# Kernel optimization log

Measured on AMD Instinct MI355X. Metric: run time of the kernel, lower is better.

## Reference

```python
import jax, jax.numpy as jnp
import numpy as np

N_NODES = 50000
EMB = 256
HEADS = 2
N_BASE_EDGES = 100000


def setup_inputs() -> dict:
    key = jax.random.key(0)
    ks = jax.random.split(key, 12)
    x = jax.random.normal(ks[0], (N_NODES, EMB), dtype=jnp.float32)
    # bipartite edges: sources in left half, targets in right half -> no self-loops
    src = jax.random.randint(ks[1], (N_BASE_EDGES,), 0, N_NODES // 2)
    dst = jax.random.randint(ks[2], (N_BASE_EDGES,), N_NODES // 2, N_NODES)
    edge_index = jnp.stack([src, dst]).astype(jnp.int64)
    hd = EMB // HEADS
    s = 0.02
    params = {
        "Wkqv": jax.random.normal(ks[3], (EMB, 3 * EMB), dtype=jnp.float32) * s,
        "bkqv": jnp.zeros((3 * EMB,), dtype=jnp.float32),
        "W1": jax.random.normal(ks[4], (2 * hd, hd), dtype=jnp.float32) * s,
        "b1": jnp.zeros((hd,), dtype=jnp.float32),
        "W2": jax.random.normal(ks[5], (hd, 1), dtype=jnp.float32) * s,
        "b2": jnp.zeros((1,), dtype=jnp.float32),
        "Wout": jax.random.normal(ks[6], (EMB, EMB), dtype=jnp.float32) * s,
        "bout": jnp.zeros((EMB,), dtype=jnp.float32),
    }
    return {"x": x, "edge_index": edge_index, **params}


def reference(x, edge_index, Wkqv, bkqv, W1, b1, W2, b2, Wout, bout):
    N, emb = x.shape
    H = HEADS
    hd = emb // H
    # MetaGNNNoEdgeAttr.forward preprocessing: make undirected + self loops.
    # Input is bipartite (no self-loops), so remove_self_loops is a no-op.
    ei = jnp.concatenate([edge_index, edge_index[::-1]], axis=1)
    loops = jnp.arange(N, dtype=edge_index.dtype)
    src = jnp.concatenate([ei[0], loops])  # j (message source)
    dst = jnp.concatenate([ei[1], loops])  # i (message target / softmax index)

    # single GNN layer (n_layers=1)
    kqv = x @ Wkqv + bkqv  # [N, 3*emb]
    q = kqv[dst, :emb].reshape(-1, H, hd)                                  # [E,H,hd]
    k = kqv[src, emb:2 * emb].reshape(-1, H, hd) / jnp.sqrt(jnp.float32(hd))
    v = kqv[src, 2 * emb:].reshape(-1, H, hd)

    h = jax.nn.relu(jnp.concatenate([k, q], axis=-1) @ W1 + b1)  # [E,H,hd]
    a = (h @ W2 + b2).squeeze(-1)                                # [E,H]

    # segment softmax over destination nodes (every node has a self-loop)
    m = jax.ops.segment_max(a, dst, num_segments=N)              # [N,H]
    ex = jnp.exp(a - m[dst])
    s = jax.ops.segment_sum(ex, dst, num_segments=N)             # [N,H]
    alpha = ex / (s[dst] + 1e-16)                                # [E,H]

    msg = (alpha[..., None] * v).reshape(-1, emb) @ Wout + bout  # [E,emb]
    out = jax.ops.segment_sum(msg, dst, num_segments=N)          # [N,emb]
    return jax.nn.relu(out) + x
```

## Files before the change

### kernel.cpp

```cpp
#include <hip/hip_runtime.h>
#include <hip/hip_bf16.h>

#define EMB 256

typedef __bf16 bf16_t;
typedef __attribute__((ext_vector_type(8))) __bf16 bf16x8;
typedef __attribute__((ext_vector_type(4))) __bf16 bf16x4;
typedef __attribute__((ext_vector_type(4))) float floatx4;

__device__ __forceinline__ int eidx(const int* __restrict__ p, int is64, long long k){
  return is64 ? p[2*k] : p[(int)k];
}
__device__ __forceinline__ void async_load16(const void* g, void* l){
  __builtin_amdgcn_global_load_lds(
      (const __attribute__((address_space(1))) unsigned int*)g,
      (__attribute__((address_space(3))) unsigned int*)l,
      16, 0, 0);
}
__device__ __forceinline__ float4 cvt4(bf16x4 v){
  return make_float4((float)v.x, (float)v.y, (float)v.z, (float)v.w);
}

__global__ void detect_kernel(const int* __restrict__ ei, int* __restrict__ flag){
  int z = (ei[1]==0) + (ei[3]==0) + (ei[5]==0) + (ei[7]==0);
  *flag = (z == 4) ? 1 : 0;
}

__global__ void cvt_x_kernel(const float* __restrict__ x, bf16_t* __restrict__ xb, int n4){
  int t = blockIdx.x*blockDim.x + threadIdx.x;
  if (t >= n4) return;
  const float4 v = *(const float4*)(x + (size_t)t*4);
  bf16x4 o = { (bf16_t)v.x, (bf16_t)v.y, (bf16_t)v.z, (bf16_t)v.w };
  *(bf16x4*)(xb + (size_t)t*4) = o;
}

__global__ void prep_weights(const float* __restrict__ Wkqv, const float* __restrict__ bkqv,
                             const float* __restrict__ W1,
                             bf16_t* __restrict__ WcombT, float* __restrict__ bcomb){
  int n = blockIdx.x * blockDim.x + threadIdx.x;
  int c = blockIdx.y;
  if (n >= 768) return;
  const float rs = rsqrtf(128.0f);
  bool isBias = (c == 256);
  const float* arow = isBias ? bkqv : (Wkqv + (size_t)c*768);
  float val;
  if (n < 256){
    int h = n >> 7, d = n & 127;
    float s = 0.f;
    for (int t = 0; t < 128; ++t)
      s = fmaf(arow[h*128 + t], W1[(size_t)(128 + t)*128 + d], s);
    val = s;
  } else {
    int r = n - 256;
    int h = r >> 8, t8 = r & 255;
    int g = t8 >> 3, half = (t8 >> 2) & 1, dd = t8 & 3;
    int d = g*4 + dd;
    if (half == 0){
      float s = 0.f;
      for (int t = 0; t < 128; ++t)
        s = fmaf(arow[256 + h*128 + t], W1[(size_t)t*128 + d], s);
      val = s * rs;
    } else {
      val = arow[512 + h*128 + d];
    }
  }
  if (isBias) bcomb[n] = val;
  else        WcombT[(size_t)n*256 + c] = (bf16_t)val;
}

__global__ void prep_wout(const float* __restrict__ W, bf16_t* __restrict__ Wt){
  int t = blockIdx.x*blockDim.x + threadIdx.x;
  int n = t & 255, c = t >> 8;
  Wt[(size_t)n*256 + c] = (bf16_t)W[(size_t)c*256 + n];
}

__global__ void deg_kernel(const int* __restrict__ ei, const int* __restrict__ flag,
                           int* __restrict__ deg, int E0, int Nn){
  int t = blockIdx.x*blockDim.x + threadIdx.x;
  if (t >= 2*E0) return;
  int is64 = *flag;
  int i = (t < E0) ? eidx(ei,is64,(long long)E0+t) : eidx(ei,is64,t-E0);
  i = min(max(i,0), Nn-1);
  atomicAdd(deg + i, 1);
}

__global__ __launch_bounds__(1024) void scan1_kernel(const int* __restrict__ deg,
                                                     int* __restrict__ off,
                                                     int* __restrict__ bsum, int N){
  __shared__ int wsum[16];
  int tid = threadIdx.x, lane = tid & 63, w = tid >> 6;
  int i = blockIdx.x*1024 + tid;
  int v = (i < N) ? (deg[i] + 1) : 0;
  int incl = v;
  #pragma unroll
  for (int o = 1; o < 64; o <<= 1){
    int t = __shfl_up(incl, o, 64);
    if (lane >= o) incl += t;
  }
  if (lane == 63) wsum[w] = incl;
  __syncthreads();
  if (w == 0 && lane < 16){
    int sv = wsum[lane];
    #pragma unroll
    for (int o = 1; o < 16; o <<= 1){
      int t = __shfl_up(sv, o, 64);
      if (lane >= o) sv += t;
    }
    wsum[lane] = sv;
  }
  __syncthreads();
  int wpref = (w == 0) ? 0 : wsum[w-1];
  if (i < N) off[i] = wpref + incl - v;
  if (tid == 1023) bsum[blockIdx.x] = wpref + incl;
}

__global__ __launch_bounds__(1024) void scan2_kernel(int* __restrict__ bsum,
                                                     int* __restrict__ off, int nb, int N){
  __shared__ int wsum[16];
  int tid = threadIdx.x, lane = tid & 63, w = tid >> 6;
  int v = (tid < nb) ? bsum[tid] : 0;
  int incl = v;
  #pragma unroll
  for (int o = 1; o < 64; o <<= 1){
    int t = __shfl_up(incl, o, 64);
    if (lane >= o) incl += t;
  }
  if (lane == 63) wsum[w] = incl;
  __syncthreads();
  if (w == 0 && lane < 16){
    int sv = wsum[lane];
    #pragma unroll
    for (int o = 1; o < 16; o <<= 1){
      int t = __shfl_up(sv, o, 64);
      if (lane >= o) sv += t;
    }
    wsum[lane] = sv;
  }
  __syncthreads();
  int wpref = (w == 0) ? 0 : wsum[w-1];
  if (tid < nb) bsum[tid] = wpref + incl - v;
  if (tid == 1023) off[N] = wpref + incl;
}

__global__ void scan3_kernel(int* __restrict__ off, const int* __restrict__ bsum, int N){
  int i = blockIdx.x*256 + threadIdx.x;
  if (i < N) off[i] += bsum[i >> 10];
}

__global__ void scatter_kernel(const int* __restrict__ ei, const int* __restrict__ flag,
                               const int* __restrict__ off, int* __restrict__ cursor,
                               int* __restrict__ bj, int E0, int Nn){
  int e = blockIdx.x*blockDim.x + threadIdx.x;
  int E = 2*E0 + Nn;
  if (e >= E) return;
  int is64 = *flag;
  int j, i;
  if (e < E0){ j = eidx(ei,is64,e); i = eidx(ei,is64,(long long)E0+e); }
  else if (e < 2*E0){ int t = e - E0; i = eidx(ei,is64,t); j = eidx(ei,is64,(long long)E0+t); }
  else { i = j = e - 2*E0; }
  i = min(max(i,0), Nn-1); j = min(max(j,0), Nn-1);
  int pos = atomicAdd(cursor + i, 1);
  bj[off[i] + pos] = j;
}

template<int MODE, typename OutT>
__global__ __launch_bounds__(256) void mfma_gemm(
    const bf16_t* __restrict__ A, const bf16_t* __restrict__ Bt,
    const float* __restrict__ bias, OutT* __restrict__ C,
    int M, int N,
    const int* __restrict__ deg, const float* __restrict__ xres)
{
  __shared__ bf16_t As[2][128*32];
  __shared__ bf16_t Bs[2][128*32];
  const int tid = threadIdx.x;
  const int wave = tid >> 6, lane = tid & 63;
  const int row16 = lane & 15, quad = lane >> 4;

  const int nn = N >> 7;
  const int bid = blockIdx.x;
  const int strip = bid / (8*nn);
  const int inner = bid % (8*nn);
  const int m0 = (strip*8 + (inner & 7)) * 128;
  const int n0 = (inner >> 3) * 128;
  const int wm = (wave >> 1) * 64, wn = (wave & 1) * 64;

  const int f0 = wave*2, f1 = wave*2 + 1;
  const int gm0 = min(m0 + f0*16 + row16, M-1);
  const int gm1 = min(m0 + f1*16 + row16, M-1);
  const int gn0 = n0 + f0*16 + row16;
  const int gn1 = n0 + f1*16 + row16;

  async_load16(A  + (size_t)gm0*256 + quad*8, (char*)As[0] + f0*1024);
  async_load16(A  + (size_t)gm1*256 + quad*8, (char*)As[0] + f1*1024);
  async_load16(Bt + (size_t)gn0*256 + quad*8, (char*)Bs[0] + f0*1024);
  async_load16(Bt + (size_t)gn1*256 + quad*8, (char*)Bs[0] + f1*1024);

  floatx4 acc[4][4];
  #pragma unroll
  for (int a=0;a<4;++a)
    #pragma unroll
    for (int b=0;b<4;++b) acc[a][b] = (floatx4){0.f,0.f,0.f,0.f};

  #pragma unroll
  for (int kt = 0; kt < 8; ++kt){
    const int cur = kt & 1, nxt = cur ^ 1;
    const int k1 = (kt+1)*32;

    __syncthreads();

    if (kt < 7){
      async_load16(A  + (size_t)gm0*256 + k1 + quad*8, (char*)As[nxt] + f0*1024);
      async_load16(A  + (size_t)gm1*256 + k1 + quad*8, (char*)As[nxt] + f1*1024);
      async_load16(Bt + (size_t)gn0*256 + k1 + quad*8, (char*)Bs[nxt] + f0*1024);
      async_load16(Bt + (size_t)gn1*256 + k1 + quad*8, (char*)Bs[nxt] + f1*1024);
    }

    bf16x8 af[4], bfr[4];
    #pragma unroll
    for (int t = 0; t < 4; ++t){
      af[t]  = *(const bf16x8*)((const char*)As[cur] + ((wm>>4)+t)*1024 + lane*16);
      bfr[t] = *(const bf16x8*)((const char*)Bs[cur] + ((wn>>4)+t)*1024 + lane*16);
    }
    #pragma unroll
    for (int mt=0;mt<4;++mt)
      #pragma unroll
      for (int nt=0;nt<4;++nt)
        acc[mt][nt] = __builtin_amdgcn_mfma_f32_16x16x32_bf16(bfr[nt], af[mt], acc[mt][nt], 0,0,0);
  }

  float4 b4[4];
  #pragma unroll
  for (int nt=0;nt<4;++nt)
    b4[nt] = *(const float4*)(bias + n0 + wn + nt*16 + quad*4);

  #pragma unroll
  for (int mt=0;mt<4;++mt){
    const int m = m0 + wm + mt*16 + row16;
    if (m >= M) continue;
    const float dg = (MODE==1) ? (float)(deg[m]+1) : 0.f;
    #pragma unroll
    for (int nt=0;nt<4;++nt){
      const int nb = n0 + wn + nt*16 + quad*4;
      if (MODE == 0){
        bf16x4 o = { (bf16_t)(acc[mt][nt][0] + b4[nt].x),
                     (bf16_t)(acc[mt][nt][1] + b4[nt].y),
                     (bf16_t)(acc[mt][nt][2] + b4[nt].z),
                     (bf16_t)(acc[mt][nt][3] + b4[nt].w) };
        *(bf16x4*)((bf16_t*)C + (size_t)m*N + nb) = o;
      } else {
        const float4 xr = *(const float4*)(xres + (size_t)m*N + nb);
        float4 o;
        o.x = fmaxf(acc[mt][nt][0] + dg*b4[nt].x, 0.f) + xr.x;
        o.y = fmaxf(acc[mt][nt][1] + dg*b4[nt].y, 0.f) + xr.y;
        o.z = fmaxf(acc[mt][nt][2] + dg*b4[nt].z, 0.f) + xr.z;
        o.w = fmaxf(acc[mt][nt][3] + dg*b4[nt].w, 0.f) + xr.w;
        *(float4*)((float*)C + (size_t)m*N + nb) = o;
      }
    }
  }
}

__device__ __forceinline__ float score4(bf16x8 kvv, float4 qv, float4 b1v, float4 w2v){
  return fmaxf(qv.x+(float)kvv[0]+b1v.x, 0.f)*w2v.x
       + fmaxf(qv.y+(float)kvv[1]+b1v.y, 0.f)*w2v.y
       + fmaxf(qv.z+(float)kvv[2]+b1v.z, 0.f)*w2v.z
       + fmaxf(qv.w+(float)kvv[3]+b1v.w, 0.f)*w2v.w;
}
__device__ __forceinline__ float hredux(float p){
  #pragma unroll
  for (int o = 16; o >= 1; o >>= 1)
    p += __shfl_xor(p, o, 64);
  return p;
}
__global__ __launch_bounds__(256) void fused_attn_kernel(
    const bf16_t* __restrict__ P, const int* __restrict__ bj, const int* __restrict__ off,
    const float* __restrict__ b1, const float* __restrict__ W2, const float* __restrict__ b2,
    bf16_t* __restrict__ aggb, int Nn)
{
  int i = blockIdx.x * (blockDim.x >> 6) + (threadIdx.x >> 6);
  if (i >= Nn) return;
  int lane = threadIdx.x & 63;
  int h = lane >> 5, g = lane & 31, d = g * 4;

  const float4 qv  = cvt4(*(const bf16x4*)(P + (size_t)i*768 + h*128 + d));
  const float4 b1v = *(const float4*)(b1 + d);
  const float4 w2v = *(const float4*)(W2 + d);
  const float b2v  = b2[0];
  const bf16_t* __restrict__ Pkv = P + 256 + h*256 + g*8;

  float m = -3.0e38f, s = 0.f;
  float4 acc = make_float4(0.f,0.f,0.f,0.f);
  const int s0 = off[i], s1 = off[i+1], s1m1 = s1 - 1;

  for (int t = s0; t < s1; t += 4){
    const int cnt = s1 - t;
    const int jA = bj[t];
    const int jB = bj[min(t+1, s1m1)];
    const int jC = bj[min(t+2, s1m1)];
    const int jD = bj[min(t+3, s1m1)];
    const bf16x8 kA = *(const bf16x8*)(Pkv + (size_t)jA*768);
    const bf16x8 kB = *(const bf16x8*)(Pkv + (size_t)jB*768);
    const bf16x8 kC = *(const bf16x8*)(Pkv + (size_t)jC*768);
    const bf16x8 kD = *(const bf16x8*)(Pkv + (size_t)jD*768);
    float pA = hredux(score4(kA, qv, b1v, w2v));
    float pB = hredux(score4(kB, qv, b1v, w2v));
    float pC = hredux(score4(kC, qv, b1v, w2v));
    float pD = hredux(score4(kD, qv, b1v, w2v));
    const float aA = pA + b2v;
    const float aB = (cnt > 1) ? pB + b2v : -3.0e38f;
    const float aC = (cnt > 2) ? pC + b2v : -3.0e38f;
    const float aD = (cnt > 3) ? pD + b2v : -3.0e38f;
    const float amax = fmaxf(fmaxf(aA, aB), fmaxf(aC, aD));
    const float mn = fmaxf(m, amax);
    const float sc = __expf(m - mn);
    const float eA = __expf(aA - mn);
    const float eB = __expf(aB - mn);
    const float eC = __expf(aC - mn);
    const float eD = __expf(aD - mn);
    s = s*sc + ((eA + eB) + (eC + eD));
    acc.x = acc.x*sc + ((eA*(float)kA[4] + eB*(float)kB[4]) + (eC*(float)kC[4] + eD*(float)kD[4]));
    acc.y = acc.y*sc + ((eA*(float)kA[5] + eB*(float)kB[5]) + (eC*(float)kC[5] + eD*(float)kD[5]));
    acc.z = acc.z*sc + ((eA*(float)kA[6] + eB*(float)kB[6]) + (eC*(float)kC[6] + eD*(float)kD[6]));
    acc.w = acc.w*sc + ((eA*(float)kA[7] + eB*(float)kB[7]) + (eC*(float)kC[7] + eD*(float)kD[7]));
    m = mn;
  }
  float inv = 1.f / (s + 1e-16f);
  bf16x4 ob = { (bf16_t)(acc.x*inv), (bf16_t)(acc.y*inv), (bf16_t)(acc.z*inv), (bf16_t)(acc.w*inv) };
  *(bf16x4*)(aggb + (size_t)i*256 + h*128 + d) = ob;
}

extern "C" void kernel_launch(void* const* d_in, const int* in_sizes, int n_in,
                              void* d_out, int out_size, void* d_ws, size_t ws_size,
                              hipStream_t stream)
{
  const float* x     = (const float*)d_in[0];
  const int*   ei    = (const int*)d_in[1];
  const float* Wkqv  = (const float*)d_in[2];
  const float* bkqv  = (const float*)d_in[3];
  const float* W1    = (const float*)d_in[4];
  const float* b1    = (const float*)d_in[5];
  const float* W2    = (const float*)d_in[6];
  const float* b2    = (const float*)d_in[7];
  const float* Wout  = (const float*)d_in[8];
  const float* bout  = (const float*)d_in[9];
  float* out = (float*)d_out;

  const int N  = in_sizes[0] / EMB;
  const int E0 = in_sizes[1] / 2;
  const int E  = 2*E0 + N;

  float* base = (float*)d_ws;
  bf16_t* WcombT = (bf16_t*)base;
  float*  bcomb  = base + 98304;
  bf16_t* WoutT  = (bf16_t*)(base + 98304 + 768);
  bf16_t* xb     = (bf16_t*)(base + 131840);
  bf16_t* Pb     = (bf16_t*)(base + 131840 + 6400000);
  bf16_t* aggb   = (bf16_t*)(Pb + (size_t)N*768);
  int* deg       = (int*)(aggb + (size_t)N*256);
  int* cursor    = deg + N;
  int* flag      = cursor + N;
  int* off       = flag + 1;
  int* bj        = off + (N+1);
  int* bsum      = (int*)aggb;

  hipMemsetAsync(deg, 0, (size_t)2*N*sizeof(int), stream);

  detect_kernel<<<1,1,0,stream>>>(ei, flag);
  cvt_x_kernel<<<((N*EMB/4)+255)/256,256,0,stream>>>(x, xb, N*EMB/4);
  prep_weights<<<dim3(3,257),256,0,stream>>>(Wkqv, bkqv, W1, WcombT, bcomb);
  prep_wout<<<256,256,0,stream>>>(Wout, WoutT);

  deg_kernel<<<(2*E0+255)/256,256,0,stream>>>(ei, flag, deg, E0, N);
  const int nb = (N + 1023)/1024;
  scan1_kernel<<<nb,1024,0,stream>>>(deg, off, bsum, N);
  scan2_kernel<<<1,1024,0,stream>>>(bsum, off, nb, N);
  scan3_kernel<<<(N+255)/256,256,0,stream>>>(off, bsum, N);
  scatter_kernel<<<(E+255)/256,256,0,stream>>>(ei, flag, off, cursor, bj, E0, N);

  const int nm8 = (((N+127)/128) + 7) & ~7;
  mfma_gemm<0, bf16_t><<<nm8*6,256,0,stream>>>(xb, WcombT, bcomb, Pb, N, 768, nullptr, nullptr);
  fused_attn_kernel<<<(N+3)/4,256,0,stream>>>(Pb, bj, off, b1, W2, b2, aggb, N);
  mfma_gemm<1, float><<<nm8*2,256,0,stream>>>(aggb, WoutT, bout, out, N, 256, deg, x);
}
```

Baseline: 293.0 us.

## Use 8-wave GEMM blocks and inline 64-bit index detection

The MFMA GEMM moves from 4 waves per 128x128 tile to 8 waves, each computing a 64x32 sub-tile. This halves per-wave accumulators and load work, aiming for more latency hiding and occupancy. The single-thread detect kernel launch is removed, and each thread in the degree and scatter kernels now checks the index width itself by reading four words. This saves one launch and serialization point, at the cost of a few redundant cached loads per thread.

```diff
diff --git a/kernel.cpp b/kernel.cpp
--- a/kernel.cpp
+++ b/kernel.cpp
@@ -20,10 +20,8 @@
 __device__ __forceinline__ float4 cvt4(bf16x4 v){
   return make_float4((float)v.x, (float)v.y, (float)v.z, (float)v.w);
 }
-
-__global__ void detect_kernel(const int* __restrict__ ei, int* __restrict__ flag){
-  int z = (ei[1]==0) + (ei[3]==0) + (ei[5]==0) + (ei[7]==0);
-  *flag = (z == 4) ? 1 : 0;
+__device__ __forceinline__ int detect64(const int* __restrict__ ei){
+  return ((ei[1] | ei[3] | ei[5] | ei[7]) == 0) ? 1 : 0;
 }
 
 __global__ void cvt_x_kernel(const float* __restrict__ x, bf16_t* __restrict__ xb, int n4){
@@ -74,11 +72,11 @@
   Wt[(size_t)n*256 + c] = (bf16_t)W[(size_t)c*256 + n];
 }
 
-__global__ void deg_kernel(const int* __restrict__ ei, const int* __restrict__ flag,
+__global__ void deg_kernel(const int* __restrict__ ei,
                            int* __restrict__ deg, int E0, int Nn){
   int t = blockIdx.x*blockDim.x + threadIdx.x;
   if (t >= 2*E0) return;
-  int is64 = *flag;
+  int is64 = detect64(ei);
   int i = (t < E0) ? eidx(ei,is64,(long long)E0+t) : eidx(ei,is64,t-E0);
   i = min(max(i,0), Nn-1);
   atomicAdd(deg + i, 1);
@@ -147,13 +145,13 @@
   if (i < N) off[i] += bsum[i >> 10];
 }
 
-__global__ void scatter_kernel(const int* __restrict__ ei, const int* __restrict__ flag,
+__global__ void scatter_kernel(const int* __restrict__ ei,
                                const int* __restrict__ off, int* __restrict__ cursor,
                                int* __restrict__ bj, int E0, int Nn){
   int e = blockIdx.x*blockDim.x + threadIdx.x;
   int E = 2*E0 + Nn;
   if (e >= E) return;
-  int is64 = *flag;
+  int is64 = detect64(ei);
   int j, i;
   if (e < E0){ j = eidx(ei,is64,e); i = eidx(ei,is64,(long long)E0+e); }
   else if (e < 2*E0){ int t = e - E0; i = eidx(ei,is64,t); j = eidx(ei,is64,(long long)E0+t); }
@@ -164,7 +162,7 @@
 }
 
 template<int MODE, typename OutT>
-__global__ __launch_bounds__(256) void mfma_gemm(
+__global__ __launch_bounds__(512, 4) void mfma_gemm(
     const bf16_t* __restrict__ A, const bf16_t* __restrict__ Bt,
     const float* __restrict__ bias, OutT* __restrict__ C,
     int M, int N,
@@ -182,24 +180,21 @@
   const int inner = bid % (8*nn);
   const int m0 = (strip*8 + (inner & 7)) * 128;
   const int n0 = (inner >> 3) * 128;
-  const int wm = (wave >> 1) * 64, wn = (wave & 1) * 64;
-
-  const int f0 = wave*2, f1 = wave*2 + 1;
+  const int wm  = (wave >> 2) * 64;
+  const int wnq = (wave & 3) * 32;
+
+  const int f0 = wave;
   const int gm0 = min(m0 + f0*16 + row16, M-1);
-  const int gm1 = min(m0 + f1*16 + row16, M-1);
   const int gn0 = n0 + f0*16 + row16;
-  const int gn1 = n0 + f1*16 + row16;
 
   async_load16(A  + (size_t)gm0*256 + quad*8, (char*)As[0] + f0*1024);
-  async_load16(A  + (size_t)gm1*256 + quad*8, (char*)As[0] + f1*1024);
   async_load16(Bt + (size_t)gn0*256 + quad*8, (char*)Bs[0] + f0*1024);
-  async_load16(Bt + (size_t)gn1*256 + quad*8, (char*)Bs[0] + f1*1024);
-
-  floatx4 acc[4][4];
+
+  floatx4 acc[4][2];
   #pragma unroll
   for (int a=0;a<4;++a)
     #pragma unroll
-    for (int b=0;b<4;++b) acc[a][b] = (floatx4){0.f,0.f,0.f,0.f};
+    for (int b=0;b<2;++b) acc[a][b] = (floatx4){0.f,0.f,0.f,0.f};
 
   #pragma unroll
   for (int kt = 0; kt < 8; ++kt){
@@ -210,28 +205,28 @@
 
     if (kt < 7){
       async_load16(A  + (size_t)gm0*256 + k1 + quad*8, (char*)As[nxt] + f0*1024);
-      async_load16(A  + (size_t)gm1*256 + k1 + quad*8, (char*)As[nxt] + f1*1024);
       async_load16(Bt + (size_t)gn0*256 + k1 + quad*8, (char*)Bs[nxt] + f0*1024);
-      async_load16(Bt + (size_t)gn1*256 + k1 + quad*8, (char*)Bs[nxt] + f1*1024);
-    }
-
-    bf16x8 af[4], bfr[4];
-    #pragma unroll
-    for (int t = 0; t < 4; ++t){
+    }
+
+    bf16x8 af[4], bfr[2];
+    #pragma unroll
+    for (int t = 0; t < 4; ++t)
       af[t]  = *(const bf16x8*)((const char*)As[cur] + ((wm>>4)+t)*1024 + lane*16);
-      bfr[t] = *(const bf16x8*)((const char*)Bs[cur] + ((wn>>4)+t)*1024 + lane*16);
-    }
+    #pragma unroll
+    for (int u = 0; u < 2; ++u)
+      bfr[u] = *(const bf16x8*)((const char*)Bs[cur] + ((wnq>>4)+u)*1024 + lane*16);
+
     #pragma unroll
     for (int mt=0;mt<4;++mt)
       #pragma unroll
-      for (int nt=0;nt<4;++nt)
+      for (int nt=0;nt<2;++nt)
         acc[mt][nt] = __builtin_amdgcn_mfma_f32_16x16x32_bf16(bfr[nt], af[mt], acc[mt][nt], 0,0,0);
   }
 
-  float4 b4[4];
-  #pragma unroll
-  for (int nt=0;nt<4;++nt)
-    b4[nt] = *(const float4*)(bias + n0 + wn + nt*16 + quad*4);
+  float4 b4[2];
+  #pragma unroll
+  for (int nt=0;nt<2;++nt)
+    b4[nt] = *(const float4*)(bias + n0 + wnq + nt*16 + quad*4);
 
   #pragma unroll
   for (int mt=0;mt<4;++mt){
@@ -239,8 +234,8 @@
     if (m >= M) continue;
     const float dg = (MODE==1) ? (float)(deg[m]+1) : 0.f;
     #pragma unroll
-    for (int nt=0;nt<4;++nt){
-      const int nb = n0 + wn + nt*16 + quad*4;
+    for (int nt=0;nt<2;++nt){
+      const int nb = n0 + wnq + nt*16 + quad*4;
       if (MODE == 0){
         bf16x4 o = { (bf16_t)(acc[mt][nt][0] + b4[nt].x),
                      (bf16_t)(acc[mt][nt][1] + b4[nt].y),
@@ -365,20 +360,19 @@
 
   hipMemsetAsync(deg, 0, (size_t)2*N*sizeof(int), stream);
 
-  detect_kernel<<<1,1,0,stream>>>(ei, flag);
   cvt_x_kernel<<<((N*EMB/4)+255)/256,256,0,stream>>>(x, xb, N*EMB/4);
   prep_weights<<<dim3(3,257),256,0,stream>>>(Wkqv, bkqv, W1, WcombT, bcomb);
   prep_wout<<<256,256,0,stream>>>(Wout, WoutT);
 
-  deg_kernel<<<(2*E0+255)/256,256,0,stream>>>(ei, flag, deg, E0, N);
+  deg_kernel<<<(2*E0+255)/256,256,0,stream>>>(ei, deg, E0, N);
   const int nb = (N + 1023)/1024;
   scan1_kernel<<<nb,1024,0,stream>>>(deg, off, bsum, N);
   scan2_kernel<<<1,1024,0,stream>>>(bsum, off, nb, N);
   scan3_kernel<<<(N+255)/256,256,0,stream>>>(off, bsum, N);
-  scatter_kernel<<<(E+255)/256,256,0,stream>>>(ei, flag, off, cursor, bj, E0, N);
+  scatter_kernel<<<(E+255)/256,256,0,stream>>>(ei, off, cursor, bj, E0, N);
 
   const int nm8 = (((N+127)/128) + 7) & ~7;
-  mfma_gemm<0, bf16_t><<<nm8*6,256,0,stream>>>(xb, WcombT, bcomb, Pb, N, 768, nullptr, nullptr);
+  mfma_gemm<0, bf16_t><<<nm8*6,512,0,stream>>>(xb, WcombT, bcomb, Pb, N, 768, nullptr, nullptr);
   fused_attn_kernel<<<(N+3)/4,256,0,stream>>>(Pb, bj, off, b1, W2, b2, aggb, N);
-  mfma_gemm<1, float><<<nm8*2,256,0,stream>>>(aggb, WoutT, bout, out, N, 256, deg, x);
-}
+  mfma_gemm<1, float><<<nm8*2,512,0,stream>>>(aggb, WoutT, bout, out, N, 256, deg, x);
+}
```

Result: no change. 292.0 us (-0.4%).
